# Kernel tuning notes

Measured on AMD Instinct MI355X. Metric: run time of the kernel, lower is better.

The kernel has to match this reference:

```python
import jax, jax.numpy as jnp
import numpy as np

N_NODES = 100000
N_EDGES = 640000
F_IN = 128
HID = 128
N_CLASSES = 10
N_GRAPHS = 64


def _sage_conv(x, src, tgt, Wl, bl, Wr, num_nodes):
    # PyG SAGEConv (mean aggr): out = lin_l(mean_{j in N(i)} x_j) + lin_r(x_i)
    msg_sum = jax.ops.segment_sum(x[src], tgt, num_segments=num_nodes)      # [N, F]
    deg = jax.ops.segment_sum(jnp.ones((src.shape[0],), x.dtype), tgt,
                              num_segments=num_nodes)                        # [N]
    agg = msg_sum / jnp.maximum(deg, 1.0)[:, None]
    return agg @ Wl + bl + x @ Wr


def setup_inputs() -> dict:
    key = jax.random.key(0)
    ks = jax.random.split(key, 12)
    def lin(k, fan_in, fan_out):
        s = 1.0 / np.sqrt(fan_in)
        return jax.random.uniform(k, (fan_in, fan_out), jnp.float32, -s, s)
    x = jax.random.normal(ks[0], (N_NODES, F_IN), jnp.float32)
    edge_index = jax.random.randint(ks[1], (2, N_EDGES), 0, N_NODES, jnp.int64)
    batch = jnp.sort(jax.random.randint(ks[2], (N_NODES,), 0, N_GRAPHS, jnp.int64))
    return {
        "x": x, "edge_index": edge_index, "batch": batch,
        "W1l": lin(ks[3], F_IN, HID), "b1": jnp.zeros((HID,), jnp.float32), "W1r": lin(ks[4], F_IN, HID),
        "W2l": lin(ks[5], HID, HID), "b2": jnp.zeros((HID,), jnp.float32), "W2r": lin(ks[6], HID, HID),
        "W3l": lin(ks[7], HID, HID), "b3": jnp.zeros((HID,), jnp.float32), "W3r": lin(ks[8], HID, HID),
        "Wout": lin(ks[9], HID, N_CLASSES), "bout": jnp.zeros((N_CLASSES,), jnp.float32),
    }


def reference(x, edge_index, batch, W1l, b1, W1r, W2l, b2, W2r, W3l, b3, W3r, Wout, bout):
    src, tgt = edge_index[0], edge_index[1]
    n = x.shape[0]
    h = jax.nn.relu(_sage_conv(x, src, tgt, W1l, b1, W1r, n))
    h = jax.nn.relu(_sage_conv(h, src, tgt, W2l, b2, W2r, n))
    h = _sage_conv(h, src, tgt, W3l, b3, W3r, n)
    # global mean pool over graphs
    g_sum = jax.ops.segment_sum(h, batch, num_segments=N_GRAPHS)            # [G, H]
    g_cnt = jax.ops.segment_sum(jnp.ones((n,), h.dtype), batch, num_segments=N_GRAPHS)
    g = g_sum / jnp.maximum(g_cnt, 1.0)[:, None]
    # dropout is identity in eval mode
    return g @ Wout + bout
```

## Files before the change

### kernel.cpp

```cpp
#include <hip/hip_runtime.h>
#include <hip/hip_bf16.h>

#define N_NODES_C 100000
#define N_GRAPHS_C 64
#define FDIM 128
#define NPB 512
#define NBUCK 196
#define SB 256
#define CAP 4096

typedef _Float16 half8v __attribute__((ext_vector_type(8)));
typedef __attribute__((ext_vector_type(4))) float f32x4;
typedef __attribute__((ext_vector_type(2))) float f32x2;

__device__ __forceinline__ unsigned short f2h(float f) {
    union { _Float16 h; unsigned short u; } v; v.h = (_Float16)f; return v.u;
}

__device__ __forceinline__ void acc8h(float* a, half8v v) {
#pragma unroll
    for (int j = 0; j < 8; ++j) a[j] += (float)v[j];
}

__device__ __forceinline__ unsigned pk4fp8(float a, float b, float c, float d) {
    int w = 0;
    w = __builtin_amdgcn_cvt_pk_fp8_f32(a, b, w, false);
    w = __builtin_amdgcn_cvt_pk_fp8_f32(c, d, w, true);
    return (unsigned)w;
}
__device__ __forceinline__ void acc16fp8(float* a, uint4 v) {
    f32x2 f;
    f = __builtin_amdgcn_cvt_pk_f32_fp8(v.x, false); a[0]  += f.x; a[1]  += f.y;
    f = __builtin_amdgcn_cvt_pk_f32_fp8(v.x, true);  a[2]  += f.x; a[3]  += f.y;
    f = __builtin_amdgcn_cvt_pk_f32_fp8(v.y, false); a[4]  += f.x; a[5]  += f.y;
    f = __builtin_amdgcn_cvt_pk_f32_fp8(v.y, true);  a[6]  += f.x; a[7]  += f.y;
    f = __builtin_amdgcn_cvt_pk_f32_fp8(v.z, false); a[8]  += f.x; a[9]  += f.y;
    f = __builtin_amdgcn_cvt_pk_f32_fp8(v.z, true);  a[10] += f.x; a[11] += f.y;
    f = __builtin_amdgcn_cvt_pk_f32_fp8(v.w, false); a[12] += f.x; a[13] += f.y;
    f = __builtin_amdgcn_cvt_pk_f32_fp8(v.w, true);  a[14] += f.x; a[15] += f.y;
}

__device__ __forceinline__ void prep_w_body(const float* __restrict__ Wl,
                                            const float* __restrict__ Wr,
                                            unsigned short* __restrict__ outW, int id) {
    int c = id >> 9, i = id & 511;
    int l = i >> 3, e = i & 7;
    int khalf = c >> 5, nf = (c >> 2) & 7, ks4 = c & 3;
    int j = nf * 16 + (l & 15);
    int k = khalf * 128 + ks4 * 32 + ((l >> 4) << 3) + e;
    float w = (k < 128) ? Wl[k * 128 + j] : Wr[(k - 128) * 128 + j];
    outW[id] = f2h(w);
}

__global__ __launch_bounds__(256) void prep_scatter(const int* __restrict__ src,
                                                    const int* __restrict__ tgt,
                                                    int* __restrict__ cur,
                                                    uint2* __restrict__ staged, int E,
                                                    const float* __restrict__ x,
                                                    unsigned short* __restrict__ B0,
                                                    unsigned char* __restrict__ B08, int n8,
                                                    const float* __restrict__ W1l,
                                                    const float* __restrict__ W1r,
                                                    unsigned short* __restrict__ wt1,
                                                    const float* __restrict__ W2l,
                                                    const float* __restrict__ W2r,
                                                    unsigned short* __restrict__ wt2,
                                                    const int* __restrict__ batch,
                                                    int* __restrict__ gstart,
                                                    float* __restrict__ gcnt,
                                                    float* __restrict__ pa,
                                                    float* __restrict__ ph,
                                                    int nNodes, int convBlocks) {
    __shared__ int lcnt[NBUCK];
    __shared__ int lbase[NBUCK];
    const int b = blockIdx.x;
    const int t = threadIdx.x;

    if (b < SB) {
        if (t < NBUCK) lcnt[t] = 0;
        __syncthreads();
        const int chunk = (E + SB - 1) / SB;
        const int base = b * chunk;
        const int lim = min(E, base + chunk);
        for (int e = base + t; e < lim; e += 256)
            atomicAdd(&lcnt[tgt[e] >> 9], 1);
        __syncthreads();
        if (t < NBUCK) {
            int c = lcnt[t];
            lbase[t] = c ? atomicAdd(&cur[t], c) : 0;
            lcnt[t] = 0;
        }
        __syncthreads();
        for (int e = base + t; e < lim; e += 256) {
            int tv = tgt[e];
            int bk = tv >> 9;
            int r = atomicAdd(&lcnt[bk], 1);
            int pos = lbase[bk] + r;
            if (pos < CAP) {
                uint2 p; p.x = (unsigned)tv; p.y = (unsigned)src[e];
                staged[(size_t)bk * CAP + pos] = p;
            }
        }
    } else if (b < SB + 128) {
        prep_w_body(W1l, W1r, wt1, (b - SB) * 256 + t);
    } else if (b < SB + 256) {
        prep_w_body(W2l, W2r, wt2, (b - SB - 128) * 256 + t);
    } else if (b < SB + 256 + convBlocks) {
        int i = (b - SB - 256) * 256 + t;
        if (i < n8) {
            float4 v0 = *(const float4*)(x + (size_t)i * 8);
            float4 v1 = *(const float4*)(x + (size_t)i * 8 + 4);
            half8v o;
            o[0] = (_Float16)v0.x; o[1] = (_Float16)v0.y; o[2] = (_Float16)v0.z; o[3] = (_Float16)v0.w;
            o[4] = (_Float16)v1.x; o[5] = (_Float16)v1.y; o[6] = (_Float16)v1.z; o[7] = (_Float16)v1.w;
            *(half8v*)(B0 + (size_t)i * 8) = o;
            uint2 p8;
            p8.x = pk4fp8(v0.x, v0.y, v0.z, v0.w);
            p8.y = pk4fp8(v1.x, v1.y, v1.z, v1.w);
            *(uint2*)(B08 + (size_t)i * 8) = p8;
        }
    } else {
        if (t < 64) {
            int g = t;
            int lo = 0, hi = nNodes;
            while (lo < hi) { int m = (lo + hi) >> 1; if (batch[m] < g) lo = m + 1; else hi = m; }
            int lb = lo;
            lo = 0; hi = nNodes;
            while (lo < hi) { int m = (lo + hi) >> 1; if (batch[m] < g + 1) lo = m + 1; else hi = m; }
            gstart[g] = lb;
            gcnt[g] = (float)(lo - lb);
            if (g == 0) gstart[64] = nNodes;
        }
        for (int i = t; i < N_GRAPHS_C * FDIM; i += 256) { pa[i] = 0.f; ph[i] = 0.f; }
    }
}

__global__ __launch_bounds__(256) void bucket_finalize(const uint2* __restrict__ staged,
                                                       const int* __restrict__ cur,
                                                       int2* __restrict__ rsbe,
                                                       float* __restrict__ invd,
                                                       int* __restrict__ csr, int N) {
    __shared__ int dcnt[NPB];
    __shared__ int pref[NPB];
    __shared__ int ts[256];
    const int t = threadIdx.x;
    const int b = blockIdx.x;
    const int s = b * CAP;
    const int e = s + min(cur[b], CAP);
    const int nb0 = b * NPB;
    const int nn = min(NPB, N - nb0);

    dcnt[t] = 0; dcnt[t + 256] = 0;
    __syncthreads();
    for (int i = s + t; i < e; i += 256)
        atomicAdd(&dcnt[(int)staged[i].x - nb0], 1);
    __syncthreads();

    int a0 = dcnt[2 * t], a1 = dcnt[2 * t + 1];
    ts[t] = a0 + a1;
    __syncthreads();
    for (int off = 1; off < 256; off <<= 1) {
        int u = (t >= off) ? ts[t - off] : 0;
        __syncthreads();
        ts[t] += u;
        __syncthreads();
    }
    int excl = (t > 0) ? ts[t - 1] : 0;
    pref[2 * t] = excl;
    pref[2 * t + 1] = excl + a0;
    __syncthreads();

    if (t < nn) {
        int bg = s + pref[t];
        rsbe[nb0 + t] = make_int2(bg, bg + dcnt[t]);
        invd[nb0 + t] = 1.0f / (float)max(dcnt[t], 1);
    }
    int t2 = t + 256;
    if (t2 < nn) {
        int bg = s + pref[t2];
        rsbe[nb0 + t2] = make_int2(bg, bg + dcnt[t2]);
        invd[nb0 + t2] = 1.0f / (float)max(dcnt[t2], 1);
    }
    __syncthreads();

    dcnt[t] = pref[t]; dcnt[t + 256] = pref[t + 256];
    __syncthreads();
    for (int i = s + t; i < e; i += 256) {
        uint2 p = staged[i];
        int r = atomicAdd(&dcnt[(int)p.x - nb0], 1);
        csr[s + r] = (int)p.y;
    }
}

__global__ __launch_bounds__(512) void sage_layer(const unsigned short* __restrict__ Xin,
                                                  const unsigned char* __restrict__ X8in,
                                                  const unsigned short* __restrict__ WtF,
                                                  const float* __restrict__ bias,
                                                  const int* __restrict__ csr,
                                                  const int2* __restrict__ rsbe,
                                                  const float* __restrict__ invd,
                                                  unsigned short* __restrict__ Hout,
                                                  unsigned char* __restrict__ H8out, int N) {
    __shared__ unsigned short atile[128 * 128];
    __shared__ unsigned short wlds[32 * 512];

    const int t = threadIdx.x;
    const int r0 = blockIdx.x * 128;

#pragma unroll
    for (int rep = 0; rep < 4; ++rep) {
        int e = rep * 4096 + t * 8;
        *(half8v*)&wlds[e] = *(const half8v*)(WtF + e);
    }

    {
        const int grp = t >> 3, lane = t & 7;
#pragma unroll
        for (int it = 0; it < 2; ++it) {
            const int row = it * 64 + grp;
            const int node = r0 + row;
            float a[16];
#pragma unroll
            for (int j = 0; j < 16; ++j) a[j] = 0.f;
            if (node < N) {
                const int2 be = rsbe[node];
                const int beg = be.x, end = be.y;
                for (int base = beg; base < end; base += 8) {
                    const int cnt = end - base;
                    int idx[8];
#pragma unroll
                    for (int k = 0; k < 8; ++k) idx[k] = csr[min(base + k, end - 1)];
                    uint4 v[8];
#pragma unroll
                    for (int k = 0; k < 8; ++k) {
                        if (k < cnt)
                            v[k] = *(const uint4*)(X8in + ((size_t)idx[k] << 7) + lane * 16);
                    }
#pragma unroll
                    for (int k = 0; k < 8; ++k) {
                        if (k < cnt) acc16fp8(a, v[k]);
                    }
                }
                float sc = invd[node];
#pragma unroll
                for (int j = 0; j < 16; ++j) a[j] *= sc;
            }
            half8v o0, o1;
#pragma unroll
            for (int j = 0; j < 8; ++j) { o0[j] = (_Float16)a[j]; o1[j] = (_Float16)a[8 + j]; }
            const int c0 = (2 * lane) ^ (row & 7);
            const int c1 = (2 * lane + 1) ^ (row & 7);
            *(half8v*)&atile[row * 128 + c0 * 8] = o0;
            *(half8v*)&atile[row * 128 + c1 * 8] = o1;
        }
    }
    __syncthreads();

    const int wave = t >> 6, l = t & 63;
    const int trow = wave * 16 + (l & 15);
    const int lk = (l >> 4) << 3;

    f32x4 acc[8];
#pragma unroll
    for (int nf = 0; nf < 8; ++nf) acc[nf] = (f32x4)(0.f);

#pragma unroll
    for (int ks4 = 0; ks4 < 4; ++ks4) {
        const int chunk = (ks4 * 4 + (l >> 4)) ^ (trow & 7);
        half8v af = *(const half8v*)&atile[trow * 128 + chunk * 8];
#pragma unroll
        for (int nf = 0; nf < 8; ++nf) {
            half8v bh = *(const half8v*)&wlds[(nf * 4 + ks4) * 512 + l * 8];
            acc[nf] = __builtin_amdgcn_mfma_f32_16x16x32_f16(bh, af, acc[nf], 0, 0, 0);
        }
    }
    __syncthreads();
#pragma unroll
    for (int rep = 0; rep < 4; ++rep) {
        int e = rep * 4096 + t * 8;
        *(half8v*)&wlds[e] = *(const half8v*)(WtF + 16384 + e);
    }
    __syncthreads();

    {
        int row = r0 + trow;
        if (row >= N) row = N - 1;
#pragma unroll
        for (int ks4 = 0; ks4 < 4; ++ks4) {
            half8v af = *(const half8v*)(Xin + ((size_t)row << 7) + ks4 * 32 + lk);
#pragma unroll
            for (int nf = 0; nf < 8; ++nf) {
                half8v bh = *(const half8v*)&wlds[(nf * 4 + ks4) * 512 + l * 8];
                acc[nf] = __builtin_amdgcn_mfma_f32_16x16x32_f16(bh, af, acc[nf], 0, 0, 0);
            }
        }
    }

    const int jb = (l >> 4) << 2;
    const int orow = r0 + trow;
    if (orow < N) {
#pragma unroll
        for (int nf = 0; nf < 8; ++nf) {
            float4 bv = *(const float4*)&bias[nf * 16 + jb];
            float o0 = fmaxf(acc[nf][0] + bv.x, 0.f);
            float o1 = fmaxf(acc[nf][1] + bv.y, 0.f);
            float o2 = fmaxf(acc[nf][2] + bv.z, 0.f);
            float o3 = fmaxf(acc[nf][3] + bv.w, 0.f);
            uint2 st;
            st.x = (unsigned)f2h(o0) | ((unsigned)f2h(o1) << 16);
            st.y = (unsigned)f2h(o2) | ((unsigned)f2h(o3) << 16);
            *(uint2*)(Hout + ((size_t)orow << 7) + nf * 16 + jb) = st;
            *(unsigned*)(H8out + ((size_t)orow << 7) + nf * 16 + jb) = pk4fp8(o0, o1, o2, o3);
        }
    }
}

__global__ __launch_bounds__(256) void agg3_pool(const unsigned short* __restrict__ H2,
                                                 const unsigned char* __restrict__ H28,
                                                 const int* __restrict__ csr,
                                                 const int2* __restrict__ rsbe,
                                                 const float* __restrict__ invd,
                                                 const int* __restrict__ gstart,
                                                 float* __restrict__ pa,
                                                 float* __restrict__ ph) {
    const int g = blockIdx.x >> 4;
    const int q = blockIdx.x & 15;
    const int s = gstart[g], e = gstart[g + 1];
    const int len = e - s;
    const int cs = s + (len * q) / 16;
    const int ce = s + (len * (q + 1)) / 16;
    const int t = threadIdx.x;
    const int grp = t >> 3, lane = t & 7;

    float aacc[16], hacc[16];
#pragma unroll
    for (int j = 0; j < 16; ++j) { aacc[j] = 0.f; hacc[j] = 0.f; }

    for (int node = cs + grp; node < ce; node += 32) {
        const int2 be = rsbe[node];
        const int beg = be.x, end = be.y;
        float a[16];
#pragma unroll
        for (int j = 0; j < 16; ++j) a[j] = 0.f;
        for (int base = beg; base < end; base += 8) {
            const int cnt = end - base;
            int idx[8];
#pragma unroll
            for (int k = 0; k < 8; ++k) idx[k] = csr[min(base + k, end - 1)];
            uint4 v[8];
#pragma unroll
            for (int k = 0; k < 8; ++k) {
                if (k < cnt)
                    v[k] = *(const uint4*)(H28 + ((size_t)idx[k] << 7) + lane * 16);
            }
#pragma unroll
            for (int k = 0; k < 8; ++k) {
                if (k < cnt) acc16fp8(a, v[k]);
            }
        }
        const float sc = invd[node];
#pragma unroll
        for (int j = 0; j < 16; ++j) aacc[j] += a[j] * sc;
        half8v own0 = *(const half8v*)(H2 + ((size_t)node << 7) + lane * 16);
        half8v own1 = *(const half8v*)(H2 + ((size_t)node << 7) + lane * 16 + 8);
        acc8h(hacc, own0);
        acc8h(hacc + 8, own1);
    }

    __shared__ float red[32][128];
#pragma unroll
    for (int j = 0; j < 16; ++j) red[grp][lane * 16 + j] = aacc[j];
    __syncthreads();
    if (t < 128) {
        float sum = 0.f;
#pragma unroll
        for (int k = 0; k < 32; ++k) sum += red[k][t];
        unsafeAtomicAdd(&pa[g * 128 + t], sum);
    }
    __syncthreads();
#pragma unroll
    for (int j = 0; j < 16; ++j) red[grp][lane * 16 + j] = hacc[j];
    __syncthreads();
    if (t < 128) {
        float sum = 0.f;
#pragma unroll
        for (int k = 0; k < 32; ++k) sum += red[k][t];
        unsafeAtomicAdd(&ph[g * 128 + t], sum);
    }
}

__global__ __launch_bounds__(128) void final_fused(const float* __restrict__ pa,
                                                   const float* __restrict__ ph,
                                                   const float* __restrict__ gcnt,
                                                   const float* __restrict__ W3l,
                                                   const float* __restrict__ W3r,
                                                   const float* __restrict__ b3,
                                                   const float* __restrict__ Wout,
                                                   const float* __restrict__ bout,
                                                   float* __restrict__ out) {
    __shared__ float sA[FDIM], sH[FDIM], sT[FDIM];
    int g = blockIdx.x;
    int j = threadIdx.x;
    float inv = 1.0f / fmaxf(gcnt[g], 1.0f);
    sA[j] = pa[g * FDIM + j] * inv;
    sH[j] = ph[g * FDIM + j] * inv;
    __syncthreads();
    float acc = b3[j];
    for (int c = 0; c < FDIM; ++c)
        acc += sA[c] * W3l[c * FDIM + j] + sH[c] * W3r[c * FDIM + j];
    sT[j] = acc;
    __syncthreads();
    if (j < 10) {
        float o = bout[j];
        for (int c = 0; c < FDIM; ++c) o += sT[c] * Wout[c * 10 + j];
        out[g * 10 + j] = o;
    }
}

extern "C" void kernel_launch(void* const* d_in, const int* in_sizes, int n_in,
                              void* d_out, int out_size, void* d_ws, size_t ws_size,
                              hipStream_t stream) {
    const float* x     = (const float*)d_in[0];
    const int*   edge  = (const int*)d_in[1];
    const int*   batch = (const int*)d_in[2];
    const float* W1l = (const float*)d_in[3];
    const float* b1  = (const float*)d_in[4];
    const float* W1r = (const float*)d_in[5];
    const float* W2l = (const float*)d_in[6];
    const float* b2  = (const float*)d_in[7];
    const float* W2r = (const float*)d_in[8];
    const float* W3l = (const float*)d_in[9];
    const float* b3  = (const float*)d_in[10];
    const float* W3r = (const float*)d_in[11];
    const float* Wout = (const float*)d_in[12];
    const float* bout = (const float*)d_in[13];
    float* out = (float*)d_out;

    const int N = N_NODES_C;
    const int E = in_sizes[1] / 2;
    const int* src = edge;
    const int* tgt = edge + E;

    char* ws = (char*)d_ws;
    size_t off = 0;
    auto carve = [&](size_t bytes) { char* p = ws + off; off += (bytes + 255) & ~(size_t)255; return p; };
    int2*  rsbe = (int2*)carve((size_t)N * 8);
    float* invd = (float*)carve((size_t)N * 4);
    int*   gstart = (int*)carve(65 * 4);
    float* gcnt = (float*)carve(64 * 4);
    float* pa   = (float*)carve((size_t)N_GRAPHS_C * FDIM * 4);
    float* ph   = (float*)carve((size_t)N_GRAPHS_C * FDIM * 4);
    int*   cur  = (int*)carve(NBUCK * 4);
    unsigned short* wt1 = (unsigned short*)carve(32768 * 2);
    unsigned short* wt2 = (unsigned short*)carve(32768 * 2);
    uint2* staged = (uint2*)carve((size_t)NBUCK * CAP * 8);
    int*   csr  = (int*)carve((size_t)NBUCK * CAP * 4);
    unsigned short* B0 = (unsigned short*)carve((size_t)N * FDIM * 2);
    unsigned short* B2 = (unsigned short*)carve((size_t)N * FDIM * 2);
    unsigned char* F0 = (unsigned char*)carve((size_t)N * FDIM);
    unsigned char* F1 = (unsigned char*)carve((size_t)N * FDIM);

    hipMemsetAsync(cur, 0, NBUCK * 4, stream);
    const int n8 = N * FDIM / 8;
    const int convBlocks = (n8 + 255) / 256;
    prep_scatter<<<SB + 256 + convBlocks + 1, 256, 0, stream>>>(
        src, tgt, cur, staged, E,
        x, B0, F0, n8,
        W1l, W1r, wt1, W2l, W2r, wt2,
        batch, gstart, gcnt, pa, ph, N, convBlocks);

    bucket_finalize<<<NBUCK, 256, 0, stream>>>(staged, cur, rsbe, invd, csr, N);

    const int layerGrid = (N + 127) / 128;

    sage_layer<<<layerGrid, 512, 0, stream>>>(B0, F0, wt1, b1, csr, rsbe, invd, B2, F1, N);
    sage_layer<<<layerGrid, 512, 0, stream>>>(B2, F1, wt2, b2, csr, rsbe, invd, B0, F0, N);

    agg3_pool<<<N_GRAPHS_C * 16, 256, 0, stream>>>(B0, F0, csr, rsbe, invd, gstart, pa, ph);

    final_fused<<<N_GRAPHS_C, 128, 0, stream>>>(pa, ph, gcnt, W3l, W3r, b3, Wout, bout, out);
}
```

Baseline: 168.8 us.

## Fuse bucket finalize into scatter kernel and final MLP into pooling via completion counters

Two kernel launches are removed. Bucket-finalize blocks now live in the prep kernel and spin on a global counter until all scatter blocks have signalled completion. The final per-graph linear layers run in the last-finishing block of the pooling kernel, detected with an atomic ticket. This saves launch gaps and tail bubbles, but it relies on the spin-waiting blocks not starving the scatter blocks. The last block also runs all 64 graphs serially, which leaves a long single-block tail.

Measured after the change: 666.5 us. 295% more time.

```diff
diff --git a/kernel.cpp b/kernel.cpp
--- a/kernel.cpp
+++ b/kernel.cpp
@@ -52,35 +52,98 @@
     outW[id] = f2h(w);
 }
 
-__global__ __launch_bounds__(256) void prep_scatter(const int* __restrict__ src,
-                                                    const int* __restrict__ tgt,
-                                                    int* __restrict__ cur,
-                                                    uint2* __restrict__ staged, int E,
-                                                    const float* __restrict__ x,
-                                                    unsigned short* __restrict__ B0,
-                                                    unsigned char* __restrict__ B08, int n8,
-                                                    const float* __restrict__ W1l,
-                                                    const float* __restrict__ W1r,
-                                                    unsigned short* __restrict__ wt1,
-                                                    const float* __restrict__ W2l,
-                                                    const float* __restrict__ W2r,
-                                                    unsigned short* __restrict__ wt2,
-                                                    const int* __restrict__ batch,
-                                                    int* __restrict__ gstart,
-                                                    float* __restrict__ gcnt,
-                                                    float* __restrict__ pa,
-                                                    float* __restrict__ ph,
-                                                    int nNodes, int convBlocks) {
-    __shared__ int lcnt[NBUCK];
-    __shared__ int lbase[NBUCK];
+__global__ __launch_bounds__(256) void prep_scatter_fin(const int* __restrict__ src,
+                                                        const int* __restrict__ tgt,
+                                                        int* __restrict__ cur,
+                                                        int* __restrict__ done,
+                                                        uint2* __restrict__ staged, int E,
+                                                        int2* __restrict__ rsbe,
+                                                        float* __restrict__ invd,
+                                                        int* __restrict__ csr,
+                                                        const float* __restrict__ x,
+                                                        unsigned short* __restrict__ B0,
+                                                        unsigned char* __restrict__ B08, int n8,
+                                                        const float* __restrict__ W1l,
+                                                        const float* __restrict__ W1r,
+                                                        unsigned short* __restrict__ wt1,
+                                                        const float* __restrict__ W2l,
+                                                        const float* __restrict__ W2r,
+                                                        unsigned short* __restrict__ wt2,
+                                                        const int* __restrict__ batch,
+                                                        int* __restrict__ gstart,
+                                                        float* __restrict__ gcnt,
+                                                        float* __restrict__ pa,
+                                                        float* __restrict__ ph,
+                                                        int N, int convBlocks) {
     const int b = blockIdx.x;
     const int t = threadIdx.x;
 
-    if (b < SB) {
+    if (b < NBUCK) {
+        __shared__ int ready;
+        if (t == 0) {
+            while (*(volatile int*)done < SB) __builtin_amdgcn_s_sleep(8);
+            ready = 1;
+        }
+        __syncthreads();
+        (void)ready;
+        __threadfence();
+
+        __shared__ int dcnt[NPB];
+        __shared__ int pref[NPB];
+        __shared__ int ts[256];
+        const int s = b * CAP;
+        const int e = s + min(cur[b], CAP);
+        const int nb0 = b * NPB;
+        const int nn = min(NPB, N - nb0);
+
+        dcnt[t] = 0; dcnt[t + 256] = 0;
+        __syncthreads();
+        for (int i = s + t; i < e; i += 256)
+            atomicAdd(&dcnt[(int)staged[i].x - nb0], 1);
+        __syncthreads();
+
+        int a0 = dcnt[2 * t], a1 = dcnt[2 * t + 1];
+        ts[t] = a0 + a1;
+        __syncthreads();
+        for (int off = 1; off < 256; off <<= 1) {
+            int u = (t >= off) ? ts[t - off] : 0;
+            __syncthreads();
+            ts[t] += u;
+            __syncthreads();
+        }
+        int excl = (t > 0) ? ts[t - 1] : 0;
+        pref[2 * t] = excl;
+        pref[2 * t + 1] = excl + a0;
+        __syncthreads();
+
+        if (t < nn) {
+            int bg = s + pref[t];
+            rsbe[nb0 + t] = make_int2(bg, bg + dcnt[t]);
+            invd[nb0 + t] = 1.0f / (float)max(dcnt[t], 1);
+        }
+        int t2 = t + 256;
+        if (t2 < nn) {
+            int bg = s + pref[t2];
+            rsbe[nb0 + t2] = make_int2(bg, bg + dcnt[t2]);
+            invd[nb0 + t2] = 1.0f / (float)max(dcnt[t2], 1);
+        }
+        __syncthreads();
+
+        dcnt[t] = pref[t]; dcnt[t + 256] = pref[t + 256];
+        __syncthreads();
+        for (int i = s + t; i < e; i += 256) {
+            uint2 p = staged[i];
+            int r = atomicAdd(&dcnt[(int)p.x - nb0], 1);
+            csr[s + r] = (int)p.y;
+        }
+    } else if (b < NBUCK + SB) {
+        __shared__ int lcnt[NBUCK];
+        __shared__ int lbase[NBUCK];
+        const int blk = b - NBUCK;
         if (t < NBUCK) lcnt[t] = 0;
         __syncthreads();
         const int chunk = (E + SB - 1) / SB;
-        const int base = b * chunk;
+        const int base = blk * chunk;
         const int lim = min(E, base + chunk);
         for (int e = base + t; e < lim; e += 256)
             atomicAdd(&lcnt[tgt[e] >> 9], 1);
@@ -101,12 +164,15 @@
                 staged[(size_t)bk * CAP + pos] = p;
             }
         }
-    } else if (b < SB + 128) {
-        prep_w_body(W1l, W1r, wt1, (b - SB) * 256 + t);
-    } else if (b < SB + 256) {
-        prep_w_body(W2l, W2r, wt2, (b - SB - 128) * 256 + t);
-    } else if (b < SB + 256 + convBlocks) {
-        int i = (b - SB - 256) * 256 + t;
+        __threadfence();
+        __syncthreads();
+        if (t == 0) atomicAdd(done, 1);
+    } else if (b < NBUCK + SB + 128) {
+        prep_w_body(W1l, W1r, wt1, (b - NBUCK - SB) * 256 + t);
+    } else if (b < NBUCK + SB + 256) {
+        prep_w_body(W2l, W2r, wt2, (b - NBUCK - SB - 128) * 256 + t);
+    } else if (b < NBUCK + SB + 256 + convBlocks) {
+        int i = (b - NBUCK - SB - 256) * 256 + t;
         if (i < n8) {
             float4 v0 = *(const float4*)(x + (size_t)i * 8);
             float4 v1 = *(const float4*)(x + (size_t)i * 8 + 4);
@@ -122,73 +188,16 @@
     } else {
         if (t < 64) {
             int g = t;
-            int lo = 0, hi = nNodes;
+            int lo = 0, hi = N;
             while (lo < hi) { int m = (lo + hi) >> 1; if (batch[m] < g) lo = m + 1; else hi = m; }
             int lb = lo;
-            lo = 0; hi = nNodes;
+            lo = 0; hi = N;
             while (lo < hi) { int m = (lo + hi) >> 1; if (batch[m] < g + 1) lo = m + 1; else hi = m; }
             gstart[g] = lb;
             gcnt[g] = (float)(lo - lb);
-            if (g == 0) gstart[64] = nNodes;
+            if (g == 0) gstart[64] = N;
         }
         for (int i = t; i < N_GRAPHS_C * FDIM; i += 256) { pa[i] = 0.f; ph[i] = 0.f; }
-    }
-}
-
-__global__ __launch_bounds__(256) void bucket_finalize(const uint2* __restrict__ staged,
-                                                       const int* __restrict__ cur,
-                                                       int2* __restrict__ rsbe,
-                                                       float* __restrict__ invd,
-                                                       int* __restrict__ csr, int N) {
-    __shared__ int dcnt[NPB];
-    __shared__ int pref[NPB];
-    __shared__ int ts[256];
-    const int t = threadIdx.x;
-    const int b = blockIdx.x;
-    const int s = b * CAP;
-    const int e = s + min(cur[b], CAP);
-    const int nb0 = b * NPB;
-    const int nn = min(NPB, N - nb0);
-
-    dcnt[t] = 0; dcnt[t + 256] = 0;
-    __syncthreads();
-    for (int i = s + t; i < e; i += 256)
-        atomicAdd(&dcnt[(int)staged[i].x - nb0], 1);
-    __syncthreads();
-
-    int a0 = dcnt[2 * t], a1 = dcnt[2 * t + 1];
-    ts[t] = a0 + a1;
-    __syncthreads();
-    for (int off = 1; off < 256; off <<= 1) {
-        int u = (t >= off) ? ts[t - off] : 0;
-        __syncthreads();
-        ts[t] += u;
-        __syncthreads();
-    }
-    int excl = (t > 0) ? ts[t - 1] : 0;
-    pref[2 * t] = excl;
-    pref[2 * t + 1] = excl + a0;
-    __syncthreads();
-
-    if (t < nn) {
-        int bg = s + pref[t];
-        rsbe[nb0 + t] = make_int2(bg, bg + dcnt[t]);
-        invd[nb0 + t] = 1.0f / (float)max(dcnt[t], 1);
-    }
-    int t2 = t + 256;
-    if (t2 < nn) {
-        int bg = s + pref[t2];
-        rsbe[nb0 + t2] = make_int2(bg, bg + dcnt[t2]);
-        invd[nb0 + t2] = 1.0f / (float)max(dcnt[t2], 1);
-    }
-    __syncthreads();
-
-    dcnt[t] = pref[t]; dcnt[t + 256] = pref[t + 256];
-    __syncthreads();
-    for (int i = s + t; i < e; i += 256) {
-        uint2 p = staged[i];
-        int r = atomicAdd(&dcnt[(int)p.x - nb0], 1);
-        csr[s + r] = (int)p.y;
     }
 }
 
@@ -315,14 +324,22 @@
     }
 }
 
-__global__ __launch_bounds__(256) void agg3_pool(const unsigned short* __restrict__ H2,
-                                                 const unsigned char* __restrict__ H28,
-                                                 const int* __restrict__ csr,
-                                                 const int2* __restrict__ rsbe,
-                                                 const float* __restrict__ invd,
-                                                 const int* __restrict__ gstart,
-                                                 float* __restrict__ pa,
-                                                 float* __restrict__ ph) {
+__global__ __launch_bounds__(256) void agg3_pool_final(const unsigned short* __restrict__ H2,
+                                                       const unsigned char* __restrict__ H28,
+                                                       const int* __restrict__ csr,
+                                                       const int2* __restrict__ rsbe,
+                                                       const float* __restrict__ invd,
+                                                       const int* __restrict__ gstart,
+                                                       float* __restrict__ pa,
+                                                       float* __restrict__ ph,
+                                                       int* __restrict__ pdone,
+                                                       const float* __restrict__ gcnt,
+                                                       const float* __restrict__ W3l,
+                                                       const float* __restrict__ W3r,
+                                                       const float* __restrict__ b3,
+                                                       const float* __restrict__ Wout,
+                                                       const float* __restrict__ bout,
+                                                       float* __restrict__ out) {
     const int g = blockIdx.x >> 4;
     const int q = blockIdx.x & 15;
     const int s = gstart[g], e = gstart[g + 1];
@@ -387,33 +404,36 @@
         for (int k = 0; k < 32; ++k) sum += red[k][t];
         unsafeAtomicAdd(&ph[g * 128 + t], sum);
     }
-}
-
-__global__ __launch_bounds__(128) void final_fused(const float* __restrict__ pa,
-                                                   const float* __restrict__ ph,
-                                                   const float* __restrict__ gcnt,
-                                                   const float* __restrict__ W3l,
-                                                   const float* __restrict__ W3r,
-                                                   const float* __restrict__ b3,
-                                                   const float* __restrict__ Wout,
-                                                   const float* __restrict__ bout,
-                                                   float* __restrict__ out) {
+
+    __shared__ int last;
+    __threadfence();
+    __syncthreads();
+    if (t == 0) last = (atomicAdd(pdone, 1) == (int)gridDim.x - 1);
+    __syncthreads();
+    if (!last) return;
+    __threadfence();
+
     __shared__ float sA[FDIM], sH[FDIM], sT[FDIM];
-    int g = blockIdx.x;
-    int j = threadIdx.x;
-    float inv = 1.0f / fmaxf(gcnt[g], 1.0f);
-    sA[j] = pa[g * FDIM + j] * inv;
-    sH[j] = ph[g * FDIM + j] * inv;
-    __syncthreads();
-    float acc = b3[j];
-    for (int c = 0; c < FDIM; ++c)
-        acc += sA[c] * W3l[c * FDIM + j] + sH[c] * W3r[c * FDIM + j];
-    sT[j] = acc;
-    __syncthreads();
-    if (j < 10) {
-        float o = bout[j];
-        for (int c = 0; c < FDIM; ++c) o += sT[c] * Wout[c * 10 + j];
-        out[g * 10 + j] = o;
+    for (int gg = 0; gg < N_GRAPHS_C; ++gg) {
+        if (t < 128) {
+            float inv = 1.0f / fmaxf(gcnt[gg], 1.0f);
+            sA[t] = pa[gg * FDIM + t] * inv;
+            sH[t] = ph[gg * FDIM + t] * inv;
+        }
+        __syncthreads();
+        if (t < 128) {
+            float acc = b3[t];
+            for (int c = 0; c < FDIM; ++c)
+                acc += sA[c] * W3l[c * FDIM + t] + sH[c] * W3r[c * FDIM + t];
+            sT[t] = acc;
+        }
+        __syncthreads();
+        if (t < 10) {
+            float o = bout[t];
+            for (int c = 0; c < FDIM; ++c) o += sT[c] * Wout[c * 10 + t];
+            out[gg * 10 + t] = o;
+        }
+        __syncthreads();
     }
 }
 
@@ -450,7 +470,9 @@
     float* gcnt = (float*)carve(64 * 4);
     float* pa   = (float*)carve((size_t)N_GRAPHS_C * FDIM * 4);
     float* ph   = (float*)carve((size_t)N_GRAPHS_C * FDIM * 4);
-    int*   cur  = (int*)carve(NBUCK * 4);
+    int*   cur  = (int*)carve((NBUCK + 2) * 4);
+    int*   done  = cur + NBUCK;
+    int*   pdone = cur + NBUCK + 1;
     unsigned short* wt1 = (unsigned short*)carve(32768 * 2);
     unsigned short* wt2 = (unsigned short*)carve(32768 * 2);
     uint2* staged = (uint2*)carve((size_t)NBUCK * CAP * 8);
@@ -460,23 +482,22 @@
     unsigned char* F0 = (unsigned char*)carve((size_t)N * FDIM);
     unsigned char* F1 = (unsigned char*)carve((size_t)N * FDIM);
 
-    hipMemsetAsync(cur, 0, NBUCK * 4, stream);
+    hipMemsetAsync(cur, 0, (NBUCK + 2) * 4, stream);
     const int n8 = N * FDIM / 8;
     const int convBlocks = (n8 + 255) / 256;
-    prep_scatter<<<SB + 256 + convBlocks + 1, 256, 0, stream>>>(
-        src, tgt, cur, staged, E,
+    prep_scatter_fin<<<NBUCK + SB + 256 + convBlocks + 1, 256, 0, stream>>>(
+        src, tgt, cur, done, staged, E,
+        rsbe, invd, csr,
         x, B0, F0, n8,
         W1l, W1r, wt1, W2l, W2r, wt2,
         batch, gstart, gcnt, pa, ph, N, convBlocks);
 
-    bucket_finalize<<<NBUCK, 256, 0, stream>>>(staged, cur, rsbe, invd, csr, N);
-
     const int layerGrid = (N + 127) / 128;
 
     sage_layer<<<layerGrid, 512, 0, stream>>>(B0, F0, wt1, b1, csr, rsbe, invd, B2, F1, N);
     sage_layer<<<layerGrid, 512, 0, stream>>>(B2, F1, wt2, b2, csr, rsbe, invd, B0, F0, N);
 
-    agg3_pool<<<N_GRAPHS_C * 16, 256, 0, stream>>>(B0, F0, csr, rsbe, invd, gstart, pa, ph);
-
-    final_fused<<<N_GRAPHS_C, 128, 0, stream>>>(pa, ph, gcnt, W3l, W3r, b3, Wout, bout, out);
-}
+    agg3_pool_final<<<N_GRAPHS_C * 16, 256, 0, stream>>>(B0, F0, csr, rsbe, invd, gstart,
+                                                         pa, ph, pdone, gcnt,
+                                                         W3l, W3r, b3, Wout, bout, out);
+}
```
